# Kernel tuning notes

Hardware: AMD Instinct MI355X
Metric: run time of the kernel (lower is better)

## Reference

```python
import jax, jax.numpy as jnp
import numpy as np

LMAX = 3
D_IRREP = (LMAX + 1) ** 2  # 16
EPS = 1e-5


def _conv1d(x, w, pad):
    # x: [N, C_in, L], w: [C_out, C_in, K] -> [N, C_out, L]
    return jax.lax.conv_general_dilated(
        x, w, window_strides=(1,), padding=[(pad, pad)],
        dimension_numbers=("NCH", "OIH", "NCH"))


def setup_inputs() -> dict:
    key = jax.random.key(0)
    ks = jax.random.split(key, 8)
    B, Cin, Cout, N, K, RES = 128, 256, 256, 64, 5, 8
    return {
        "x": jax.random.normal(ks[0], (B, Cin * D_IRREP, N), jnp.float32),
        "weight": jax.random.normal(ks[1], (LMAX + 1, Cout, Cin, K), jnp.float32) / np.sqrt(Cin * K).astype(np.float32),
        "bias": jax.random.normal(ks[2], (1, 1, Cout), jnp.float32) * 0.02,
        "affine_weight": jnp.ones((LMAX + 1, Cout), jnp.float32),
        "gating_w": jax.random.normal(ks[3], (Cout, Cout), jnp.float32) / np.sqrt(Cout).astype(np.float32),
        "gating_b": jnp.zeros((Cout,), jnp.float32),
        "to_grid": jax.random.normal(ks[4], (RES, RES, D_IRREP), jnp.float32) * 0.3,
        "from_grid": jax.random.normal(ks[5], (RES, RES, D_IRREP), jnp.float32) * 0.3,
    }


def reference(x, weight, bias, affine_weight, gating_w, gating_b, to_grid, from_grid):
    B, CI, N = x.shape
    Cin = CI // D_IRREP
    Cout = weight.shape[1]
    pad = weight.shape[-1] // 2
    x = x.reshape(B, Cin, D_IRREP, N)

    # per-degree Conv1d over the time axis, irrep order folded into batch
    h_parts = []
    for l in range(LMAX + 1):
        lo, li = l * l, 2 * l + 1
        x_l = x[:, :, lo:lo + li, :]                                  # [B, Cin, li, N]
        x_l = x_l.transpose(0, 2, 1, 3).reshape(B * li, Cin, N)       # (b i) c n
        h_l = _conv1d(x_l, weight[l], pad)                            # [B*li, Cout, N]
        h_l = h_l.reshape(B, li, Cout, N).transpose(0, 3, 1, 2).reshape(B * N, li, Cout)  # (b n) i c
        if l == 0:
            h_l = h_l + bias
        h_parts.append(h_l)
    h = jnp.concatenate(h_parts, axis=1)                              # [B*N, 16, Cout]

    # rms_norm_sh: center l=0 over channels, degree-balanced RMS, per-degree affine
    degrees = np.repeat(np.arange(LMAX + 1), 2 * np.arange(LMAX + 1) + 1)  # [16]
    bal = jnp.asarray((1.0 / (2.0 * degrees + 1.0)) / (LMAX + 1), h.dtype)  # [16]
    mean0 = jnp.mean(h[:, :1, :], axis=2, keepdims=True)
    h = jnp.concatenate([h[:, :1, :] - mean0, h[:, 1:, :]], axis=1)
    var = jnp.einsum("zic,i->zc", h * h, bal)                         # [Z, C]
    inv = jax.lax.rsqrt(jnp.mean(var, axis=-1)[:, None, None] + EPS)  # [Z,1,1]
    h = h * inv * affine_weight[degrees][None]                        # [Z,16,C]

    # SeparableS2Activation: SiLU-gated scalars + S2 grid activation for l>0
    gate = jax.nn.silu(h[:, :1, :] @ gating_w.T + gating_b)           # [Z,1,C]
    grid = jax.nn.silu(jnp.einsum("bai,zic->zbac", to_grid, h))       # [Z,8,8,C]
    s2 = jnp.einsum("bai,zbac->zic", from_grid, grid)                 # [Z,16,C]
    h = jnp.concatenate([gate, s2[:, 1:, :]], axis=1)

    # (b n) i c -> b (c i) n
    out = h.reshape(B, N, D_IRREP, Cout).transpose(0, 3, 2, 1).reshape(B, Cout * D_IRREP, N)
    return out
```

## Files before the change

### kernel.cpp

```cpp
#include <hip/hip_runtime.h>
#include <hip/hip_bf16.h>

#define BB    128
#define CIN   256
#define COUT  256
#define NN    64
#define KW    5
#define DIRR  16
#define ZTOT  (BB*NN)
#define SX    264

typedef __attribute__((ext_vector_type(4))) float f32x4;
typedef __attribute__((ext_vector_type(8))) short s16x8;

__device__ inline ushort f2bf(float f) {
    __hip_bfloat16 h = __float2bfloat16(f);
    return *(const ushort*)&h;
}
__device__ inline float bf2f(ushort u) {
    union { unsigned int ui; float f; } cv; cv.ui = ((unsigned int)u) << 16;
    return cv.f;
}
__device__ inline float wave_sum(float v) {
    #pragma unroll
    for (int o = 32; o > 0; o >>= 1) v += __shfl_down(v, o, 64);
    return v;
}
__device__ inline float silu(float x) { return x / (1.f + __expf(-x)); }

__global__ __launch_bounds__(256) void pack_all_k(const float* __restrict__ w,
                                                  const float* __restrict__ gw,
                                                  const float* __restrict__ tg,
                                                  const float* __restrict__ fg,
                                                  ushort* __restrict__ wb,
                                                  ushort* __restrict__ gwb,
                                                  ushort* __restrict__ tgb,
                                                  ushort* __restrict__ fgTb)
{
    int idx = blockIdx.x * 256 + threadIdx.x;
    if (idx < 1310720) {
        int cl = idx & 31;
        int c  = (idx >> 5) & 255;
        int ch = (idx >> 13) & 7;
        int k  = (idx >> 16) % 5;
        int l  = idx / 327680;
        int cin = ch * 32 + cl;
        wb[idx] = f2bf(w[(((size_t)(l * COUT + c) * CIN) + cin) * KW + k]);
        return;
    }
    int j2 = idx - 1310720;
    if (j2 < 65536) {
        gwb[j2] = f2bf(gw[j2]);
    } else if (j2 < 66560) {
        int j = j2 - 65536;
        tgb[j] = f2bf(tg[j]);
    } else if (j2 < 67584) {
        int j = j2 - 66560;
        int p = j >> 4, i = j & 15;
        fgTb[i * 64 + p] = f2bf(fg[j]);
    }
}

__global__ __launch_bounds__(256, 4) void conv_mfma_k(const float* __restrict__ x,
                                                      const ushort* __restrict__ wb,
                                                      const float* __restrict__ bias,
                                                      ushort* __restrict__ hbuf)
{
    __shared__ __align__(16) ushort xs[68 * SX];

    const int tid  = threadIdx.x;
    const int lane = tid & 63;
    const int wid  = tid >> 6;
    const int blk  = blockIdx.x;
    const int b = blk >> 4, i = blk & 15;
    const int l = (i == 0) ? 0 : (i < 4) ? 1 : (i < 9) ? 2 : 3;

    {
        const float4* xb = (const float4*)(x + (((size_t)b * CIN) * DIRR + i) * NN);
        #pragma unroll
        for (int p = 0; p < 16; ++p) {
            int cin = (tid & 63) | ((p & 3) << 6);
            int nq  = ((tid >> 6) << 2) | (p >> 2);
            float4 v = xb[(size_t)cin * (DIRR * NN / 4) + nq];
            ushort* dst = xs + (size_t)(2 + nq * 4) * SX + cin;
            dst[0]      = f2bf(v.x);
            dst[SX]     = f2bf(v.y);
            dst[2 * SX] = f2bf(v.z);
            dst[3 * SX] = f2bf(v.w);
        }
        xs[ 0 * SX + tid] = 0; xs[ 1 * SX + tid] = 0;
        xs[66 * SX + tid] = 0; xs[67 * SX + tid] = 0;
    }
    __syncthreads();

    f32x4 acc[4][4];
    #pragma unroll
    for (int m = 0; m < 4; ++m)
        #pragma unroll
        for (int j = 0; j < 4; ++j) acc[m][j] = (f32x4){0.f, 0.f, 0.f, 0.f};

    const int kb = lane >> 4;
    const int lr = lane & 15;

    const ushort* wl = wb + (size_t)l * (40 * 8192);
    int boffB[4];
    #pragma unroll
    for (int j = 0; j < 4; ++j)
        boffB[j] = (wid * 64 + j * 16 + lr) * 32 + kb * 8;

    const ushort* arow = xs + (size_t)lr * SX + kb * 8;

    s16x8 bva[4], bvb[4];
    {
        const ushort* bt = wl;
        #pragma unroll
        for (int j = 0; j < 4; ++j) bva[j] = *(const s16x8*)(bt + boffB[j]);
    }

    #pragma unroll 1
    for (int t = 0; t < 40; t += 2) {
        {
            const ushort* bt = wl + ((size_t)(t + 1) << 13);
            #pragma unroll
            for (int j = 0; j < 4; ++j) bvb[j] = *(const s16x8*)(bt + boffB[j]);
        }
        {
            const ushort* ab = arow + (size_t)(t >> 3) * SX + (t & 7) * 32;
            s16x8 av[4];
            #pragma unroll
            for (int m = 0; m < 4; ++m)
                av[m] = *(const s16x8*)(ab + (size_t)m * 16 * SX);
            #pragma unroll
            for (int m = 0; m < 4; ++m)
                #pragma unroll
                for (int j = 0; j < 4; ++j)
                    acc[m][j] = __builtin_amdgcn_mfma_f32_16x16x32_bf16(av[m], bva[j], acc[m][j], 0, 0, 0);
        }
        if (t + 2 < 40) {
            const ushort* bt = wl + ((size_t)(t + 2) << 13);
            #pragma unroll
            for (int j = 0; j < 4; ++j) bva[j] = *(const s16x8*)(bt + boffB[j]);
        }
        {
            int t1 = t + 1;
            const ushort* ab = arow + (size_t)(t1 >> 3) * SX + (t1 & 7) * 32;
            s16x8 av[4];
            #pragma unroll
            for (int m = 0; m < 4; ++m)
                av[m] = *(const s16x8*)(ab + (size_t)m * 16 * SX);
            #pragma unroll
            for (int m = 0; m < 4; ++m)
                #pragma unroll
                for (int j = 0; j < 4; ++j)
                    acc[m][j] = __builtin_amdgcn_mfma_f32_16x16x32_bf16(av[m], bvb[j], acc[m][j], 0, 0, 0);
        }
    }

    const int row0 = (lane >> 4) * 4;
    #pragma unroll
    for (int j = 0; j < 4; ++j) {
        int c = wid * 64 + j * 16 + lr;
        float bvv = (i == 0) ? bias[c] : 0.f;
        #pragma unroll
        for (int m = 0; m < 4; ++m)
            #pragma unroll
            for (int r = 0; r < 4; ++r) {
                int n = m * 16 + row0 + r;
                size_t z = (size_t)b * NN + n;
                hbuf[(z * DIRR + i) * COUT + c] = f2bf(acc[m][j][r] + bvv);
            }
    }
}

__global__ __launch_bounds__(256) void norm_k(const ushort* __restrict__ hbuf,
                                              const float* __restrict__ afw,
                                              ushort* __restrict__ hn2,
                                              ushort* __restrict__ hn0)
{
    __shared__ float red[16];
    const int z0 = blockIdx.x * 4;
    const int c = threadIdx.x;
    const int lane = c & 63, w = c >> 6;

    float hv[4][16];
    #pragma unroll
    for (int zz = 0; zz < 4; ++zz)
        #pragma unroll
        for (int i = 0; i < 16; ++i)
            hv[zz][i] = bf2f(hbuf[((size_t)(z0 + zz) * DIRR + i) * COUT + c]);

    float s[4];
    #pragma unroll
    for (int zz = 0; zz < 4; ++zz) s[zz] = wave_sum(hv[zz][0]);
    if (lane == 0) {
        #pragma unroll
        for (int zz = 0; zz < 4; ++zz) red[zz * 4 + w] = s[zz];
    }
    __syncthreads();
    #pragma unroll
    for (int zz = 0; zz < 4; ++zz) {
        float m = (red[zz * 4] + red[zz * 4 + 1] + red[zz * 4 + 2] + red[zz * 4 + 3]) * (1.f / 256.f);
        hv[zz][0] -= m;
    }

    const float bal[4] = {0.25f, 1.f / 12.f, 1.f / 20.f, 1.f / 28.f};
    float var[4];
    #pragma unroll
    for (int zz = 0; zz < 4; ++zz) {
        float v = bal[0] * hv[zz][0] * hv[zz][0];
        #pragma unroll
        for (int i = 1; i < 16; ++i) {
            int li = (i < 4) ? 1 : (i < 9) ? 2 : 3;
            v += bal[li] * hv[zz][i] * hv[zz][i];
        }
        var[zz] = wave_sum(v);
    }
    __syncthreads();
    if (lane == 0) {
        #pragma unroll
        for (int zz = 0; zz < 4; ++zz) red[zz * 4 + w] = var[zz];
    }
    __syncthreads();
    float inv[4];
    #pragma unroll
    for (int zz = 0; zz < 4; ++zz)
        inv[zz] = rsqrtf((red[zz * 4] + red[zz * 4 + 1] + red[zz * 4 + 2] + red[zz * 4 + 3]) * (1.f / 256.f) + 1e-5f);

    float a0 = afw[c], a1 = afw[COUT + c], a2 = afw[2 * COUT + c], a3 = afw[3 * COUT + c];
    #pragma unroll
    for (int zz = 0; zz < 4; ++zz) {
        s16x8 o0, o1;
        #pragma unroll
        for (int i = 0; i < 16; ++i) {
            float al = (i == 0) ? a0 : (i < 4) ? a1 : (i < 9) ? a2 : a3;
            ushort ub = f2bf(hv[zz][i] * inv[zz] * al);
            if (i < 8) o0[i] = (short)ub; else o1[i - 8] = (short)ub;
        }
        ushort* dst = hn2 + ((size_t)c * ZTOT + z0 + zz) * DIRR;
        *(s16x8*)dst = o0;
        *(s16x8*)(dst + 8) = o1;
        hn0[(size_t)(z0 + zz) * COUT + c] = (ushort)(unsigned short)o0[0];
    }
}

__global__ __launch_bounds__(256) void gate_k(const ushort* __restrict__ hn0,
                                              const ushort* __restrict__ gwb,
                                              const float* __restrict__ gb,
                                              float* __restrict__ out)
{
    const int b = blockIdx.x;
    const int tid = threadIdx.x;
    const int lane = tid & 63, w = tid >> 6;
    const int lr = lane & 15, kb = lane >> 4;

    f32x4 acc[4][4];
    #pragma unroll
    for (int m = 0; m < 4; ++m)
        #pragma unroll
        for (int n = 0; n < 4; ++n) acc[m][n] = (f32x4){0.f, 0.f, 0.f, 0.f};

    #pragma unroll 1
    for (int ks = 0; ks < 8; ++ks) {
        s16x8 av[4], bv[4];
        #pragma unroll
        for (int m = 0; m < 4; ++m)
            av[m] = *(const s16x8*)(hn0 + ((size_t)(b * 64 + m * 16 + lr) * 256 + ks * 32 + kb * 8));
        #pragma unroll
        for (int n = 0; n < 4; ++n)
            bv[n] = *(const s16x8*)(gwb + ((size_t)(w * 64 + n * 16 + lr) * 256 + ks * 32 + kb * 8));
        #pragma unroll
        for (int m = 0; m < 4; ++m)
            #pragma unroll
            for (int n = 0; n < 4; ++n)
                acc[m][n] = __builtin_amdgcn_mfma_f32_16x16x32_bf16(av[m], bv[n], acc[m][n], 0, 0, 0);
    }

    #pragma unroll
    for (int n = 0; n < 4; ++n) {
        int c = w * 64 + n * 16 + lr;
        float gbc = gb[c];
        #pragma unroll
        for (int m = 0; m < 4; ++m)
            #pragma unroll
            for (int r = 0; r < 4; ++r) {
                int nrow = m * 16 + kb * 4 + r;
                out[((size_t)b * COUT + c) * (DIRR * NN) + nrow] = silu(acc[m][n][r] + gbc);
            }
    }
}

__global__ __launch_bounds__(256) void grid_k(const ushort* __restrict__ hn2,
                                              const ushort* __restrict__ tgb,
                                              const ushort* __restrict__ fgTb,
                                              float* __restrict__ out)
{
    __shared__ __align__(16) char lds[36864 + 2048 + 2304];
    ushort* P_s  = (ushort*)lds;
    float*  S_s  = (float*)lds;
    ushort* tg_s = (ushort*)(lds + 36864);
    ushort* fgT_s= (ushort*)(lds + 36864 + 2048);

    const int bid = blockIdx.x;
    const int c  = bid & 255;
    const int zt = bid >> 8;
    const int z0 = zt * 256;
    const int tid = threadIdx.x;
    const int lane = tid & 63, w = tid >> 6;
    const int lr = lane & 15, kb = lane >> 4;

    #pragma unroll
    for (int q = 0; q < 4; ++q) {
        int idx = q * 256 + tid;
        tg_s[idx] = tgb[idx];
        int i = idx >> 6, p = idx & 63;
        fgT_s[i * 72 + p] = fgTb[idx];
    }
    __syncthreads();

    f32x4 acc[4][4];
    #pragma unroll
    for (int m = 0; m < 4; ++m)
        #pragma unroll
        for (int n = 0; n < 4; ++n) acc[m][n] = (f32x4){0.f, 0.f, 0.f, 0.f};

    s16x8 bv[4];
    #pragma unroll
    for (int n = 0; n < 4; ++n)
        bv[n] = (kb < 2) ? *(const s16x8*)(tg_s + (n * 16 + lr) * 16 + kb * 8)
                         : (s16x8){0,0,0,0,0,0,0,0};
    #pragma unroll
    for (int m = 0; m < 4; ++m) {
        int zl = w * 64 + m * 16 + lr;
        s16x8 av = (kb < 2) ? *(const s16x8*)(hn2 + ((size_t)c * ZTOT + z0 + zl) * DIRR + kb * 8)
                            : (s16x8){0,0,0,0,0,0,0,0};
        #pragma unroll
        for (int n = 0; n < 4; ++n)
            acc[m][n] = __builtin_amdgcn_mfma_f32_16x16x32_bf16(av, bv[n], acc[m][n], 0, 0, 0);
    }

    #pragma unroll
    for (int m = 0; m < 4; ++m)
        #pragma unroll
        for (int n = 0; n < 4; ++n)
            #pragma unroll
            for (int r = 0; r < 4; ++r) {
                int zl = w * 64 + m * 16 + kb * 4 + r;
                int p  = n * 16 + lr;
                P_s[zl * 72 + p] = f2bf(silu(acc[m][n][r]));
            }

    f32x4 acc2[4];
    #pragma unroll
    for (int m = 0; m < 4; ++m) acc2[m] = (f32x4){0.f, 0.f, 0.f, 0.f};
    #pragma unroll
    for (int ks = 0; ks < 2; ++ks) {
        s16x8 bv2 = *(const s16x8*)(fgT_s + lr * 72 + ks * 32 + kb * 8);
        #pragma unroll
        for (int m = 0; m < 4; ++m) {
            s16x8 av2 = *(const s16x8*)(P_s + (w * 64 + m * 16 + lr) * 72 + ks * 32 + kb * 8);
            acc2[m] = __builtin_amdgcn_mfma_f32_16x16x32_bf16(av2, bv2, acc2[m], 0, 0, 0);
        }
    }

    __syncthreads();

    #pragma unroll
    for (int m = 0; m < 4; ++m)
        #pragma unroll
        for (int r = 0; r < 4; ++r) {
            int zl = w * 64 + m * 16 + kb * 4 + r;
            S_s[zl * 17 + lr] = acc2[m][r];
        }
    __syncthreads();

    const int bb = tid >> 6, n = tid & 63;
    const int b0 = zt * 4;
    const float* srow = S_s + (bb * 64 + n) * 17;
    float* obase = out + ((size_t)(b0 + bb) * COUT + c) * (DIRR * NN) + n;
    #pragma unroll
    for (int i = 1; i < 16; ++i)
        obase[i * NN] = srow[i];
}

__global__ __launch_bounds__(256) void post_k(const ushort* __restrict__ hbuf,
                                              const float* __restrict__ afw,
                                              const float* __restrict__ gw,
                                              const float* __restrict__ gb,
                                              const float* __restrict__ tg,
                                              const float* __restrict__ fg,
                                              float* __restrict__ out)
{
    __shared__ float h0s[COUT];
    __shared__ float red[4];
    __shared__ float tgs[64 * 16];
    __shared__ float fgs[64 * 16];

    int z = blockIdx.x;
    int c = threadIdx.x;
    int b = z >> 6, n = z & 63;
    int lane = c & 63, wid = c >> 6;

    for (int idx = c; idx < 1024; idx += 256) { tgs[idx] = tg[idx]; fgs[idx] = fg[idx]; }

    float hv[16];
    #pragma unroll
    for (int i = 0; i < 16; ++i)
        hv[i] = bf2f(hbuf[((size_t)z * DIRR + i) * COUT + c]);

    float s0 = wave_sum(hv[0]);
    if (lane == 0) red[wid] = s0;
    __syncthreads();
    float mean0 = (red[0] + red[1] + red[2] + red[3]) * (1.f / 256.f);
    hv[0] -= mean0;

    const float bal[4] = {0.25f, 1.f / 12.f, 1.f / 20.f, 1.f / 28.f};
    float var = bal[0] * hv[0] * hv[0];
    #pragma unroll
    for (int i = 1; i < 16; ++i) {
        int li = (i < 4) ? 1 : (i < 9) ? 2 : 3;
        var += bal[li] * hv[i] * hv[i];
    }
    float s1 = wave_sum(var);
    __syncthreads();
    if (lane == 0) red[wid] = s1;
    __syncthreads();
    float inv = rsqrtf((red[0] + red[1] + red[2] + red[3]) * (1.f / 256.f) + 1e-5f);

    float a0 = afw[c], a1 = afw[COUT + c], a2 = afw[2 * COUT + c], a3 = afw[3 * COUT + c];
    #pragma unroll
    for (int i = 0; i < 16; ++i) {
        float al = (i == 0) ? a0 : (i < 4) ? a1 : (i < 9) ? a2 : a3;
        hv[i] *= inv * al;
    }
    h0s[c] = hv[0];
    __syncthreads();

    float g = gb[c];
    const float4* gwr = (const float4*)(gw + (size_t)c * COUT);
    #pragma unroll 4
    for (int j = 0; j < 64; ++j) {
        float4 wv = gwr[j];
        g += h0s[4 * j] * wv.x + h0s[4 * j + 1] * wv.y + h0s[4 * j + 2] * wv.z + h0s[4 * j + 3] * wv.w;
    }
    float gate = silu(g);

    float s2a[16];
    #pragma unroll
    for (int i = 0; i < 16; ++i) s2a[i] = 0.f;
    #pragma unroll 1
    for (int p = 0; p < 64; ++p) {
        float gv = 0.f;
        #pragma unroll
        for (int i = 0; i < 16; ++i) gv += tgs[p * 16 + i] * hv[i];
        gv = silu(gv);
        #pragma unroll
        for (int i = 0; i < 16; ++i) s2a[i] += fgs[p * 16 + i] * gv;
    }

    float* ob = out + (size_t)b * COUT * DIRR * NN + (size_t)c * DIRR * NN + n;
    ob[0] = gate;
    #pragma unroll
    for (int i = 1; i < 16; ++i) ob[i * NN] = s2a[i];
}

extern "C" void kernel_launch(void* const* d_in, const int* in_sizes, int n_in,
                              void* d_out, int out_size, void* d_ws, size_t ws_size,
                              hipStream_t stream)
{
    const float* x    = (const float*)d_in[0];
    const float* w    = (const float*)d_in[1];
    const float* bias = (const float*)d_in[2];
    const float* afw  = (const float*)d_in[3];
    const float* gw   = (const float*)d_in[4];
    const float* gb   = (const float*)d_in[5];
    const float* tg   = (const float*)d_in[6];
    const float* fg   = (const float*)d_in[7];
    float* out = (float*)d_out;

    const size_t off_hbuf = 0;
    const size_t off_wb   = 67108864;
    const size_t off_hn2  = 69730304;
    const size_t off_hn0  = off_hn2 + 67108864;
    const size_t off_gwb  = off_hn0 + 4194304;
    const size_t off_tgb  = off_gwb + 131072;
    const size_t off_fgT  = off_tgb + 2048;
    const size_t need     = off_fgT + 2048;

    ushort* hbuf = (ushort*)((char*)d_ws + off_hbuf);
    ushort* wb   = (ushort*)((char*)d_ws + off_wb);

    if (ws_size >= need) {
        ushort* hn2  = (ushort*)((char*)d_ws + off_hn2);
        ushort* hn0  = (ushort*)((char*)d_ws + off_hn0);
        ushort* gwb  = (ushort*)((char*)d_ws + off_gwb);
        ushort* tgb  = (ushort*)((char*)d_ws + off_tgb);
        ushort* fgTb = (ushort*)((char*)d_ws + off_fgT);

        pack_all_k <<<5384, 256, 0, stream>>>(w, gw, tg, fg, wb, gwb, tgb, fgTb);
        conv_mfma_k<<<BB * DIRR, 256, 0, stream>>>(x, wb, bias, hbuf);
        norm_k     <<<ZTOT / 4, 256, 0, stream>>>(hbuf, afw, hn2, hn0);
        gate_k     <<<BB, 256, 0, stream>>>(hn0, gwb, gb, out);
        grid_k     <<<256 * (ZTOT / 256), 256, 0, stream>>>(hn2, tgb, fgTb, out);
    } else {
        ushort* gwb  = wb;
        (void)gwb;
        pack_all_k <<<5120, 256, 0, stream>>>(w, gw, tg, fg, wb,
                                              (ushort*)((char*)d_ws + off_wb),
                                              (ushort*)((char*)d_ws + off_wb),
                                              (ushort*)((char*)d_ws + off_wb));
        conv_mfma_k<<<BB * DIRR, 256, 0, stream>>>(x, wb, bias, hbuf);
        post_k     <<<ZTOT, 256, 0, stream>>>(hbuf, afw, gw, gb, tg, fg, out);
    }
}
```

Before: 254.0 us.

## Deepen conv weight prefetch and process four channels per grid block

The conv kernel's B-operand prefetch goes from double to quadruple buffering, keeping three weight tiles in flight ahead of the MFMA step to better hide global load latency. The grid kernel now handles four output channels per block in a loop, cutting the block count by four and amortising the per-block loading of the to/from grid tables into LDS. This costs extra registers in the conv kernel, which may lower occupancy, and adds barriers inside the grid kernel loop.

```diff
diff --git a/kernel.cpp b/kernel.cpp
--- a/kernel.cpp
+++ b/kernel.cpp
@@ -110,50 +110,39 @@
 
     const ushort* arow = xs + (size_t)lr * SX + kb * 8;
 
-    s16x8 bva[4], bvb[4];
-    {
-        const ushort* bt = wl;
-        #pragma unroll
-        for (int j = 0; j < 4; ++j) bva[j] = *(const s16x8*)(bt + boffB[j]);
-    }
+    auto loadB = [&](s16x8* dst, int t) {
+        const ushort* bt = wl + ((size_t)t << 13);
+        #pragma unroll
+        for (int j = 0; j < 4; ++j) dst[j] = *(const s16x8*)(bt + boffB[j]);
+    };
+    auto mstep = [&](const s16x8* bv, int t) {
+        const ushort* ab = arow + (size_t)(t >> 3) * SX + (t & 7) * 32;
+        s16x8 av[4];
+        #pragma unroll
+        for (int m = 0; m < 4; ++m)
+            av[m] = *(const s16x8*)(ab + (size_t)m * 16 * SX);
+        #pragma unroll
+        for (int m = 0; m < 4; ++m)
+            #pragma unroll
+            for (int j = 0; j < 4; ++j)
+                acc[m][j] = __builtin_amdgcn_mfma_f32_16x16x32_bf16(av[m], bv[j], acc[m][j], 0, 0, 0);
+    };
+
+    s16x8 bvA[4], bvB[4], bvC[4], bvD[4];
+    loadB(bvA, 0);
+    loadB(bvB, 1);
+    loadB(bvC, 2);
 
     #pragma unroll 1
-    for (int t = 0; t < 40; t += 2) {
-        {
-            const ushort* bt = wl + ((size_t)(t + 1) << 13);
-            #pragma unroll
-            for (int j = 0; j < 4; ++j) bvb[j] = *(const s16x8*)(bt + boffB[j]);
-        }
-        {
-            const ushort* ab = arow + (size_t)(t >> 3) * SX + (t & 7) * 32;
-            s16x8 av[4];
-            #pragma unroll
-            for (int m = 0; m < 4; ++m)
-                av[m] = *(const s16x8*)(ab + (size_t)m * 16 * SX);
-            #pragma unroll
-            for (int m = 0; m < 4; ++m)
-                #pragma unroll
-                for (int j = 0; j < 4; ++j)
-                    acc[m][j] = __builtin_amdgcn_mfma_f32_16x16x32_bf16(av[m], bva[j], acc[m][j], 0, 0, 0);
-        }
-        if (t + 2 < 40) {
-            const ushort* bt = wl + ((size_t)(t + 2) << 13);
-            #pragma unroll
-            for (int j = 0; j < 4; ++j) bva[j] = *(const s16x8*)(bt + boffB[j]);
-        }
-        {
-            int t1 = t + 1;
-            const ushort* ab = arow + (size_t)(t1 >> 3) * SX + (t1 & 7) * 32;
-            s16x8 av[4];
-            #pragma unroll
-            for (int m = 0; m < 4; ++m)
-                av[m] = *(const s16x8*)(ab + (size_t)m * 16 * SX);
-            #pragma unroll
-            for (int m = 0; m < 4; ++m)
-                #pragma unroll
-                for (int j = 0; j < 4; ++j)
-                    acc[m][j] = __builtin_amdgcn_mfma_f32_16x16x32_bf16(av[m], bvb[j], acc[m][j], 0, 0, 0);
-        }
+    for (int t = 0; t < 40; t += 4) {
+        loadB(bvD, t + 3);
+        mstep(bvA, t);
+        if (t + 4 < 40) loadB(bvA, t + 4);
+        mstep(bvB, t + 1);
+        if (t + 5 < 40) loadB(bvB, t + 5);
+        mstep(bvC, t + 2);
+        if (t + 6 < 40) loadB(bvC, t + 6);
+        mstep(bvD, t + 3);
     }
 
     const int row0 = (lane >> 4) * 4;
@@ -301,8 +290,8 @@
     ushort* fgT_s= (ushort*)(lds + 36864 + 2048);
 
     const int bid = blockIdx.x;
-    const int c  = bid & 255;
-    const int zt = bid >> 8;
+    const int cg = bid & 63;
+    const int zt = bid >> 6;
     const int z0 = zt * 256;
     const int tid = threadIdx.x;
     const int lane = tid & 63, w = tid >> 6;
@@ -317,69 +306,77 @@
     }
     __syncthreads();
 
-    f32x4 acc[4][4];
-    #pragma unroll
-    for (int m = 0; m < 4; ++m)
-        #pragma unroll
-        for (int n = 0; n < 4; ++n) acc[m][n] = (f32x4){0.f, 0.f, 0.f, 0.f};
-
     s16x8 bv[4];
     #pragma unroll
     for (int n = 0; n < 4; ++n)
         bv[n] = (kb < 2) ? *(const s16x8*)(tg_s + (n * 16 + lr) * 16 + kb * 8)
                          : (s16x8){0,0,0,0,0,0,0,0};
-    #pragma unroll
-    for (int m = 0; m < 4; ++m) {
-        int zl = w * 64 + m * 16 + lr;
-        s16x8 av = (kb < 2) ? *(const s16x8*)(hn2 + ((size_t)c * ZTOT + z0 + zl) * DIRR + kb * 8)
-                            : (s16x8){0,0,0,0,0,0,0,0};
-        #pragma unroll
-        for (int n = 0; n < 4; ++n)
-            acc[m][n] = __builtin_amdgcn_mfma_f32_16x16x32_bf16(av, bv[n], acc[m][n], 0, 0, 0);
-    }
-
-    #pragma unroll
-    for (int m = 0; m < 4; ++m)
-        #pragma unroll
-        for (int n = 0; n < 4; ++n)
+
+    #pragma unroll 1
+    for (int cc = 0; cc < 4; ++cc) {
+        const int c = cg * 4 + cc;
+
+        f32x4 acc[4][4];
+        #pragma unroll
+        for (int m = 0; m < 4; ++m)
+            #pragma unroll
+            for (int n = 0; n < 4; ++n) acc[m][n] = (f32x4){0.f, 0.f, 0.f, 0.f};
+
+        #pragma unroll
+        for (int m = 0; m < 4; ++m) {
+            int zl = w * 64 + m * 16 + lr;
+            s16x8 av = (kb < 2) ? *(const s16x8*)(hn2 + ((size_t)c * ZTOT + z0 + zl) * DIRR + kb * 8)
+                                : (s16x8){0,0,0,0,0,0,0,0};
+            #pragma unroll
+            for (int n = 0; n < 4; ++n)
+                acc[m][n] = __builtin_amdgcn_mfma_f32_16x16x32_bf16(av, bv[n], acc[m][n], 0, 0, 0);
+        }
+
+        #pragma unroll
+        for (int m = 0; m < 4; ++m)
+            #pragma unroll
+            for (int n = 0; n < 4; ++n)
+                #pragma unroll
+                for (int r = 0; r < 4; ++r) {
+                    int zl = w * 64 + m * 16 + kb * 4 + r;
+                    int p  = n * 16 + lr;
+                    P_s[zl * 72 + p] = f2bf(silu(acc[m][n][r]));
+                }
+
+        f32x4 acc2[4];
+        #pragma unroll
+        for (int m = 0; m < 4; ++m) acc2[m] = (f32x4){0.f, 0.f, 0.f, 0.f};
+        #pragma unroll
+        for (int ks = 0; ks < 2; ++ks) {
+            s16x8 bv2 = *(const s16x8*)(fgT_s + lr * 72 + ks * 32 + kb * 8);
+            #pragma unroll
+            for (int m = 0; m < 4; ++m) {
+                s16x8 av2 = *(const s16x8*)(P_s + (w * 64 + m * 16 + lr) * 72 + ks * 32 + kb * 8);
+                acc2[m] = __builtin_amdgcn_mfma_f32_16x16x32_bf16(av2, bv2, acc2[m], 0, 0, 0);
+            }
+        }
+
+        __syncthreads();
+
+        #pragma unroll
+        for (int m = 0; m < 4; ++m)
             #pragma unroll
             for (int r = 0; r < 4; ++r) {
                 int zl = w * 64 + m * 16 + kb * 4 + r;
-                int p  = n * 16 + lr;
-                P_s[zl * 72 + p] = f2bf(silu(acc[m][n][r]));
+                S_s[zl * 17 + lr] = acc2[m][r];
             }
-
-    f32x4 acc2[4];
-    #pragma unroll
-    for (int m = 0; m < 4; ++m) acc2[m] = (f32x4){0.f, 0.f, 0.f, 0.f};
-    #pragma unroll
-    for (int ks = 0; ks < 2; ++ks) {
-        s16x8 bv2 = *(const s16x8*)(fgT_s + lr * 72 + ks * 32 + kb * 8);
-        #pragma unroll
-        for (int m = 0; m < 4; ++m) {
-            s16x8 av2 = *(const s16x8*)(P_s + (w * 64 + m * 16 + lr) * 72 + ks * 32 + kb * 8);
-            acc2[m] = __builtin_amdgcn_mfma_f32_16x16x32_bf16(av2, bv2, acc2[m], 0, 0, 0);
-        }
-    }
-
-    __syncthreads();
-
-    #pragma unroll
-    for (int m = 0; m < 4; ++m)
-        #pragma unroll
-        for (int r = 0; r < 4; ++r) {
-            int zl = w * 64 + m * 16 + kb * 4 + r;
-            S_s[zl * 17 + lr] = acc2[m][r];
-        }
-    __syncthreads();
-
-    const int bb = tid >> 6, n = tid & 63;
-    const int b0 = zt * 4;
-    const float* srow = S_s + (bb * 64 + n) * 17;
-    float* obase = out + ((size_t)(b0 + bb) * COUT + c) * (DIRR * NN) + n;
-    #pragma unroll
-    for (int i = 1; i < 16; ++i)
-        obase[i * NN] = srow[i];
+        __syncthreads();
+
+        const int bb = tid >> 6, n = tid & 63;
+        const int b0 = zt * 4;
+        const float* srow = S_s + (bb * 64 + n) * 17;
+        float* obase = out + ((size_t)(b0 + bb) * COUT + c) * (DIRR * NN) + n;
+        #pragma unroll
+        for (int i = 1; i < 16; ++i)
+            obase[i * NN] = srow[i];
+
+        __syncthreads();
+    }
 }
 
 __global__ __launch_bounds__(256) void post_k(const ushort* __restrict__ hbuf,
@@ -500,10 +497,8 @@
         conv_mfma_k<<<BB * DIRR, 256, 0, stream>>>(x, wb, bias, hbuf);
         norm_k     <<<ZTOT / 4, 256, 0, stream>>>(hbuf, afw, hn2, hn0);
         gate_k     <<<BB, 256, 0, stream>>>(hn0, gwb, gb, out);
-        grid_k     <<<256 * (ZTOT / 256), 256, 0, stream>>>(hn2, tgb, fgTb, out);
+        grid_k     <<<64 * (ZTOT / 256), 256, 0, stream>>>(hn2, tgb, fgTb, out);
     } else {
-        ushort* gwb  = wb;
-        (void)gwb;
         pack_all_k <<<5120, 256, 0, stream>>>(w, gw, tg, fg, wb,
                                               (ushort*)((char*)d_ws + off_wb),
                                               (ushort*)((char*)d_ws + off_wb),
```

After: 500.8 us. +97.1%, slower.

## Fuse gating GEMM into norm kernel via LDS-staged scalar rows

Applied to the files above, without the earlier changes.

Removes the separate gate kernel and the hn0 intermediate buffer by computing the SiLU-gated scalar projection inside the norm kernel. The normalized l=0 values are staged in shared memory, padded to 16 rows, and multiplied by the gate weights with MFMA. This saves a launch and a global round trip. In exchange, every block re-reads the full gate weight matrix, and 75% of the MFMA rows are zero padding.

```diff
diff --git a/kernel.cpp b/kernel.cpp
--- a/kernel.cpp
+++ b/kernel.cpp
@@ -174,13 +174,23 @@
 
 __global__ __launch_bounds__(256) void norm_k(const ushort* __restrict__ hbuf,
                                               const float* __restrict__ afw,
+                                              const ushort* __restrict__ gwb,
+                                              const float* __restrict__ gb,
                                               ushort* __restrict__ hn2,
-                                              ushort* __restrict__ hn0)
+                                              float* __restrict__ out)
 {
     __shared__ float red[16];
+    __shared__ __align__(16) ushort h0s[16 * 264];
     const int z0 = blockIdx.x * 4;
     const int c = threadIdx.x;
     const int lane = c & 63, w = c >> 6;
+    const int lr = lane & 15, kb = lane >> 4;
+
+    #pragma unroll
+    for (int q = 0; q < 17; ++q) {
+        int idx = q * 256 + c;
+        if (idx < 16 * 264) h0s[idx] = 0;
+    }
 
     float hv[4][16];
     #pragma unroll
@@ -239,53 +249,32 @@
         ushort* dst = hn2 + ((size_t)c * ZTOT + z0 + zz) * DIRR;
         *(s16x8*)dst = o0;
         *(s16x8*)(dst + 8) = o1;
-        hn0[(size_t)(z0 + zz) * COUT + c] = (ushort)(unsigned short)o0[0];
-    }
-}
-
-__global__ __launch_bounds__(256) void gate_k(const ushort* __restrict__ hn0,
-                                              const ushort* __restrict__ gwb,
-                                              const float* __restrict__ gb,
-                                              float* __restrict__ out)
-{
-    const int b = blockIdx.x;
-    const int tid = threadIdx.x;
-    const int lane = tid & 63, w = tid >> 6;
-    const int lr = lane & 15, kb = lane >> 4;
-
-    f32x4 acc[4][4];
-    #pragma unroll
-    for (int m = 0; m < 4; ++m)
-        #pragma unroll
-        for (int n = 0; n < 4; ++n) acc[m][n] = (f32x4){0.f, 0.f, 0.f, 0.f};
-
-    #pragma unroll 1
+        h0s[zz * 264 + c] = (ushort)(unsigned short)o0[0];
+    }
+    __syncthreads();
+
+    f32x4 gacc[4];
+    #pragma unroll
+    for (int j = 0; j < 4; ++j) gacc[j] = (f32x4){0.f, 0.f, 0.f, 0.f};
+    #pragma unroll
     for (int ks = 0; ks < 8; ++ks) {
-        s16x8 av[4], bv[4];
-        #pragma unroll
-        for (int m = 0; m < 4; ++m)
-            av[m] = *(const s16x8*)(hn0 + ((size_t)(b * 64 + m * 16 + lr) * 256 + ks * 32 + kb * 8));
-        #pragma unroll
-        for (int n = 0; n < 4; ++n)
-            bv[n] = *(const s16x8*)(gwb + ((size_t)(w * 64 + n * 16 + lr) * 256 + ks * 32 + kb * 8));
-        #pragma unroll
-        for (int m = 0; m < 4; ++m)
-            #pragma unroll
-            for (int n = 0; n < 4; ++n)
-                acc[m][n] = __builtin_amdgcn_mfma_f32_16x16x32_bf16(av[m], bv[n], acc[m][n], 0, 0, 0);
-    }
-
-    #pragma unroll
-    for (int n = 0; n < 4; ++n) {
-        int c = w * 64 + n * 16 + lr;
-        float gbc = gb[c];
-        #pragma unroll
-        for (int m = 0; m < 4; ++m)
-            #pragma unroll
-            for (int r = 0; r < 4; ++r) {
-                int nrow = m * 16 + kb * 4 + r;
-                out[((size_t)b * COUT + c) * (DIRR * NN) + nrow] = silu(acc[m][n][r] + gbc);
-            }
+        s16x8 ga = *(const s16x8*)(h0s + lr * 264 + ks * 32 + kb * 8);
+        #pragma unroll
+        for (int j = 0; j < 4; ++j) {
+            s16x8 gbv = *(const s16x8*)(gwb + ((size_t)(w * 64 + j * 16 + lr) * 256 + ks * 32 + kb * 8));
+            gacc[j] = __builtin_amdgcn_mfma_f32_16x16x32_bf16(ga, gbv, gacc[j], 0, 0, 0);
+        }
+    }
+    if (kb == 0) {
+        int bb = z0 >> 6, n0 = z0 & 63;
+        #pragma unroll
+        for (int j = 0; j < 4; ++j) {
+            int cp = w * 64 + j * 16 + lr;
+            float g0 = gb[cp];
+            #pragma unroll
+            for (int r = 0; r < 4; ++r)
+                out[((size_t)bb * COUT + cp) * (DIRR * NN) + (n0 + r)] = silu(gacc[j][r] + g0);
+        }
     }
 }
 
@@ -491,19 +480,15 @@
 
     if (ws_size >= need) {
         ushort* hn2  = (ushort*)((char*)d_ws + off_hn2);
-        ushort* hn0  = (ushort*)((char*)d_ws + off_hn0);
         ushort* gwb  = (ushort*)((char*)d_ws + off_gwb);
         ushort* tgb  = (ushort*)((char*)d_ws + off_tgb);
         ushort* fgTb = (ushort*)((char*)d_ws + off_fgT);
 
         pack_all_k <<<5384, 256, 0, stream>>>(w, gw, tg, fg, wb, gwb, tgb, fgTb);
         conv_mfma_k<<<BB * DIRR, 256, 0, stream>>>(x, wb, bias, hbuf);
-        norm_k     <<<ZTOT / 4, 256, 0, stream>>>(hbuf, afw, hn2, hn0);
-        gate_k     <<<BB, 256, 0, stream>>>(hn0, gwb, gb, out);
+        norm_k     <<<ZTOT / 4, 256, 0, stream>>>(hbuf, afw, gwb, gb, hn2, out);
         grid_k     <<<256 * (ZTOT / 256), 256, 0, stream>>>(hn2, tgb, fgTb, out);
     } else {
-        ushort* gwb  = wb;
-        (void)gwb;
         pack_all_k <<<5120, 256, 0, stream>>>(w, gw, tg, fg, wb,
                                               (ushort*)((char*)d_ws + off_wb),
                                               (ushort*)((char*)d_ws + off_wb),
```

After: 267.1 us. +5.1%, slower.
